# Kernel tuning notes

Hardware: AMD Instinct MI355X
Metric: run time of the kernel (lower is better)

The kernel has to match this reference:

```python
import jax, jax.numpy as jnp
import numpy as np

N = 50000
E = 800000
IN_DIM = 128
HID = 32
HEADS = 8
OUT_DIM = 64
BN_EPS = 1e-5
NEG_SLOPE = 0.2


def batch_norm(x, gamma, beta, mean, var):
    # eval-mode BatchNorm1d using running statistics
    return (x - mean) * jax.lax.rsqrt(var + BN_EPS) * gamma + beta


def gat_conv(x, src, dst, W, att_src, att_dst, heads, out_ch, n):
    """PyG GATConv (shared src/dst lin), self-loops already included in src/dst.
    x: [n, in]; W: [in, heads*out_ch]; att_*: [heads, out_ch].
    Returns [n, heads, out_ch]."""
    h = (x @ W).reshape(n, heads, out_ch)                       # node features per head
    a_s = jnp.einsum('nho,ho->nh', h, att_src)                  # [n, heads]
    a_d = jnp.einsum('nho,ho->nh', h, att_dst)
    e = jax.nn.leaky_relu(a_s[src] + a_d[dst], NEG_SLOPE)       # [e, heads]
    # segment softmax over incoming edges of each dst node
    mx = jax.ops.segment_max(e, dst, num_segments=n)
    ex = jnp.exp(e - mx[dst])
    denom = jax.ops.segment_sum(ex, dst, num_segments=n)
    alpha = ex / (denom[dst] + 1e-16)                           # [e, heads]
    out = jax.ops.segment_sum(alpha[:, :, None] * h[src], dst, num_segments=n)
    return out                                                  # [n, heads, out_ch]


def setup_inputs() -> dict:
    key = jax.random.key(0)
    ks = jax.random.split(key, 24)
    inp = {}
    inp['x'] = jax.random.normal(ks[0], (N, IN_DIM), dtype=jnp.float32)
    inp['edge_index'] = jax.random.randint(ks[1], (2, E), 0, N, dtype=jnp.int64)
    s = 0.05
    inp['W1'] = jax.random.normal(ks[2], (IN_DIM, HEADS * HID), dtype=jnp.float32) * s
    inp['a_src1'] = jax.random.normal(ks[3], (HEADS, HID), dtype=jnp.float32) * s
    inp['a_dst1'] = jax.random.normal(ks[4], (HEADS, HID), dtype=jnp.float32) * s
    inp['b1'] = jnp.zeros((HEADS * HID,), dtype=jnp.float32)
    inp['W2'] = jax.random.normal(ks[5], (HEADS * HID, OUT_DIM), dtype=jnp.float32) * s
    inp['a_src2'] = jax.random.normal(ks[6], (1, OUT_DIM), dtype=jnp.float32) * s
    inp['a_dst2'] = jax.random.normal(ks[7], (1, OUT_DIM), dtype=jnp.float32) * s
    inp['b2'] = jnp.zeros((OUT_DIM,), dtype=jnp.float32)
    # projection Linear(out_dim -> in_dim)
    inp['Wp'] = jax.random.normal(ks[8], (OUT_DIM, IN_DIM), dtype=jnp.float32) * s
    inp['bp'] = jnp.zeros((IN_DIM,), dtype=jnp.float32)
    # BatchNorm params (eval mode running stats)
    for i, d in [(1, HEADS * HID), (2, OUT_DIM), (3, IN_DIM)]:
        k0, k1, k2, k3 = jax.random.split(ks[8 + i], 4)
        inp[f'g{i}'] = 1.0 + 0.1 * jax.random.normal(k0, (d,), dtype=jnp.float32)
        inp[f'be{i}'] = 0.1 * jax.random.normal(k1, (d,), dtype=jnp.float32)
        inp[f'm{i}'] = 0.1 * jax.random.normal(k2, (d,), dtype=jnp.float32)
        inp[f'v{i}'] = jax.random.uniform(k3, (d,), dtype=jnp.float32, minval=0.5, maxval=1.5)
    return inp


def reference(x, edge_index, W1, a_src1, a_dst1, b1, W2, a_src2, a_dst2, b2,
              Wp, bp, g1, be1, m1, v1, g2, be2, m2, v2, g3, be3, m3, v3):
    n = x.shape[0]
    loops = jnp.arange(n, dtype=edge_index.dtype)
    src = jnp.concatenate([edge_index[0], loops])   # add_self_loops=True (PyG default)
    dst = jnp.concatenate([edge_index[1], loops])

    h = gat_conv(x, src, dst, W1, a_src1, a_dst1, HEADS, HID, n)
    h = h.reshape(n, HEADS * HID) + b1              # concat=True
    h = jax.nn.elu(batch_norm(h, g1, be1, m1, v1))  # dropout is no-op in eval

    h = gat_conv(h, src, dst, W2, a_src2, a_dst2, 1, OUT_DIM, n)
    h = h.reshape(n, OUT_DIM) + b2                  # concat=False, heads=1 -> mean == identity
    h = jax.nn.elu(batch_norm(h, g2, be2, m2, v2))

    h = h @ Wp + bp
    return batch_norm(h, g3, be3, m3, v3)
```

## Files before the change

### kernel.cpp

```cpp
#include <hip/hip_runtime.h>
#include <math.h>

#define NEG_SLOPE 0.2f
#define BN_EPS 1e-5f

typedef __bf16 bf16x8 __attribute__((ext_vector_type(8)));
typedef float  f32x4  __attribute__((ext_vector_type(4)));

__device__ __forceinline__ float elu_f(float x){ return x > 0.f ? x : expm1f(x); }
__device__ __forceinline__ float lrelu_f(float x){ return x > 0.f ? x : NEG_SLOPE * x; }

__device__ __forceinline__ float b2f(ushort u){
    union { uint i; float f; } v; v.i = (uint)u << 16; return v.f;
}
__device__ __forceinline__ ushort f2b(float f){
    union { float f; uint i; } v; v.f = f;
    uint r = v.i + 0x7FFFu + ((v.i >> 16) & 1u);
    return (ushort)(r >> 16);
}

__device__ __forceinline__ bool detect_f64(const void* ei, int E, long long N)
{
    const long long* p = (const long long*)ei;
    int lane = threadIdx.x & 63;
    long long v = p[lane % max(1, min(2 * E, 64))];
    bool bad = (v < 0 || v >= N);
    return __ballot(bad) == 0ull;
}

__device__ __forceinline__ void get_edge(const void* ei, int e, int E, bool f64, int& s, int& d)
{
    if (e < E) {
        if (f64) { const long long* p = (const long long*)ei; s = (int)p[e]; d = (int)p[E + e]; }
        else     { const int*       p = (const int*)ei;       s = p[e];      d = p[E + e]; }
    } else {
        s = d = e - E;
    }
}

__global__ void setup_kernel(const void* ei, int E, int N, int* deg, int cx,
    const float* __restrict__ x, ushort* __restrict__ xb,
    const float* __restrict__ W1, const float* __restrict__ W2, const float* __restrict__ Wp,
    ushort* __restrict__ wt1, ushort* __restrict__ wt2, ushort* __restrict__ wtp,
    const float* b1, const float* b2, const float* bp,
    const float* g1, const float* be1, const float* m1, const float* v1,
    const float* g2, const float* be2, const float* m2, const float* v2,
    const float* g3, const float* be3, const float* m3, const float* v3,
    float* par)
{
    int b = blockIdx.x, t = threadIdx.x;
    if (b == 0) {
        { float s = g1[t] * rsqrtf(v1[t] + BN_EPS); par[t] = s;        par[256 + t] = b1[t] * s + be1[t] - m1[t] * s; }
        if (t < 64)  { float s = g2[t] * rsqrtf(v2[t] + BN_EPS); par[512 + t] = s;  par[576 + t] = b2[t] * s + be2[t] - m2[t] * s; }
        if (t < 128) { float s = g3[t] * rsqrtf(v3[t] + BN_EPS); par[640 + t] = s;  par[768 + t] = bp[t] * s + be3[t] - m3[t] * s; }
    } else if (b <= 224) {
        int idx = (b - 1) * 256 + t;
        if (idx < 32768) {
            int n = idx >> 7, k = idx & 127;
            wt1[idx] = f2b(W1[k * 256 + n]);
        } else if (idx < 49152) {
            int j = idx - 32768;
            int n = j >> 8, k = j & 255;
            wt2[j] = f2b(W2[k * 64 + n]);
        } else if (idx < 57344) {
            int j = idx - 49152;
            int n = j >> 6, k = j & 63;
            wtp[j] = f2b(Wp[k * 128 + n]);
        }
    } else if (b < 225 + cx) {
        long long n128 = (long long)N * 128;
        long long idx = ((long long)(b - 225) * 256 + t) * 8;
        if (idx + 7 < n128) {
            float4 v0 = *reinterpret_cast<const float4*>(&x[idx]);
            float4 v1 = *reinterpret_cast<const float4*>(&x[idx + 4]);
            ushort o[8] = { f2b(v0.x), f2b(v0.y), f2b(v0.z), f2b(v0.w),
                            f2b(v1.x), f2b(v1.y), f2b(v1.z), f2b(v1.w) };
            uint4 pk;
            pk.x = (uint)o[0] | ((uint)o[1] << 16);
            pk.y = (uint)o[2] | ((uint)o[3] << 16);
            pk.z = (uint)o[4] | ((uint)o[5] << 16);
            pk.w = (uint)o[6] | ((uint)o[7] << 16);
            *reinterpret_cast<uint4*>(&xb[idx]) = pk;
        } else {
            for (long long q = idx; q < n128; ++q) xb[q] = f2b(x[q]);
        }
    } else {
        bool f64 = detect_f64(ei, E, (long long)N);
        int i = (b - 225 - cx) * 256 + t;
        int ET = E + N;
        if (i < ET) {
            int s, d;
            get_edge(ei, i, E, f64, s, d);
            atomicAdd(&deg[d], 1);
        }
    }
}

__global__ void scan1_kernel(const int* __restrict__ deg, int N, int* __restrict__ bsum)
{
    int b = blockIdx.x, t = threadIdx.x;
    int base = b * 4096 + t * 16;
    int s = 0;
    #pragma unroll
    for (int k = 0; k < 16; k += 4) {
        int idx = base + k;
        if (idx + 3 < N) {
            int4 v = *reinterpret_cast<const int4*>(&deg[idx]);
            s += v.x + v.y + v.z + v.w;
        } else {
            for (int q = 0; q < 4; ++q) if (idx + q < N) s += deg[idx + q];
        }
    }
    #pragma unroll
    for (int off = 1; off < 64; off <<= 1) s += __shfl_xor(s, off);
    __shared__ int wsum[4];
    if ((t & 63) == 0) wsum[t >> 6] = s;
    __syncthreads();
    if (t == 0) bsum[b] = wsum[0] + wsum[1] + wsum[2] + wsum[3];
}

__global__ void scan2_kernel(const int* __restrict__ bsum, int nb, int* __restrict__ bpre)
{
    if (threadIdx.x == 0) {
        int r = 0;
        for (int i = 0; i < nb; ++i) { bpre[i] = r; r += bsum[i]; }
        bpre[nb] = r;
    }
}

__global__ void scan3_kernel(const int* __restrict__ deg, int N,
                             const int* __restrict__ bpre, int nb,
                             int* __restrict__ rowptr, int* __restrict__ fillptr)
{
    int b = blockIdx.x, t = threadIdx.x;
    int base = b * 4096 + t * 16;
    int loc[16];
    int s = 0;
    #pragma unroll
    for (int k = 0; k < 16; ++k) {
        int idx = base + k;
        int d = (idx < N) ? deg[idx] : 0;
        loc[k] = s; s += d;
    }
    int lane = t & 63;
    int incl = s;
    #pragma unroll
    for (int off = 1; off < 64; off <<= 1) {
        int v = __shfl_up(incl, off);
        if (lane >= off) incl += v;
    }
    __shared__ int wsum[4];
    if (lane == 63) wsum[t >> 6] = incl;
    __syncthreads();
    int woff = 0;
    int w = t >> 6;
    for (int i = 0; i < w; ++i) woff += wsum[i];
    int off0 = bpre[b] + woff + incl - s;
    #pragma unroll
    for (int k = 0; k < 16; ++k) {
        int idx = base + k;
        if (idx < N) { rowptr[idx] = off0 + loc[k]; fillptr[idx] = off0 + loc[k]; }
    }
    if (b == 0 && t == 0) rowptr[N] = bpre[nb];
}

__global__ void fill_kernel(const void* ei, int E, int N, int* fillptr, int* esrc)
{
    bool f64 = detect_f64(ei, E, (long long)N);
    int i = blockIdx.x * blockDim.x + threadIdx.x;
    int ET = E + N;
    if (i >= ET) return;
    int s, d;
    get_edge(ei, i, E, f64, s, d);
    int pos = atomicAdd(&fillptr[d], 1);
    esrc[pos] = s;
}

__global__ void prefill_kernel(const char* __restrict__ base, int N, int NS)
{
    int k = blockIdx.x & 7;
    int s = k & (NS - 1);
    int g = blockIdx.x >> 3;
    int ngrp = gridDim.x >> 3;
    size_t slab = (size_t)N * 64;
    size_t per = (slab + ngrp - 1) / ngrp;
    size_t b0 = (size_t)g * per;
    size_t b1 = b0 + per; if (b1 > slab) b1 = slab;
    const char* p = base + (size_t)s * slab;
    uint acc = 0;
    for (size_t o = b0 + (size_t)threadIdx.x * 16; o < b1; o += (size_t)blockDim.x * 16) {
        uint4 v = *reinterpret_cast<const uint4*>(p + o);
        acc ^= v.x ^ v.y ^ v.z ^ v.w;
    }
    asm volatile("" :: "v"(acc));
}

template<int ATYPE, int OMODE, int ATT>
__global__ __launch_bounds__(256) void mgemm_kernel(const void* __restrict__ Ap,
    const ushort* __restrict__ Bt, void* __restrict__ Cp, int M, int K, int NC,
    const float* __restrict__ S, const float* __restrict__ Cc,
    const float* __restrict__ att_s, const float* __restrict__ att_d,
    float* __restrict__ as_out, float* __restrict__ ad_out)
{
    const int BM = 128, LDA = 72;
    __shared__ __align__(16) ushort As[BM][LDA];
    __shared__ __align__(16) ushort Bs[64][LDA];
    __shared__ float red[128][2];
    int t = threadIdx.x;
    int m0 = blockIdx.x * BM, n0 = blockIdx.y * 64;
    int w = t >> 6, l = t & 63;
    int wm = w >> 1, wn = w & 1;
    int r16 = l & 15, kg = l >> 4;

    f32x4 acc[4][2];
    #pragma unroll
    for (int mi = 0; mi < 4; ++mi)
        #pragma unroll
        for (int ni = 0; ni < 2; ++ni)
            acc[mi][ni] = (f32x4){0.f, 0.f, 0.f, 0.f};

    for (int kb = 0; kb < K; kb += 64) {
        if (ATYPE == 0) {
            const float* A = (const float*)Ap;
            #pragma unroll
            for (int p = 0; p < 8; ++p) {
                int r = (t >> 4) + p * 16, c4 = (t & 15) * 4;
                int gm = m0 + r;
                float4 v = (gm < M) ? *reinterpret_cast<const float4*>(&A[(size_t)gm * K + kb + c4])
                                    : make_float4(0.f, 0.f, 0.f, 0.f);
                ushort4 u; u.x = f2b(v.x); u.y = f2b(v.y); u.z = f2b(v.z); u.w = f2b(v.w);
                *reinterpret_cast<ushort4*>(&As[r][c4]) = u;
            }
        } else {
            const ushort* A = (const ushort*)Ap;
            #pragma unroll
            for (int p = 0; p < 4; ++p) {
                int r = (t >> 3) + p * 32, c8 = (t & 7) * 8;
                int gm = m0 + r;
                uint4 v = (gm < M) ? *reinterpret_cast<const uint4*>(&A[(size_t)gm * K + kb + c8])
                                   : make_uint4(0u, 0u, 0u, 0u);
                *reinterpret_cast<uint4*>(&As[r][c8]) = v;
            }
        }
        #pragma unroll
        for (int p = 0; p < 2; ++p) {
            int r = (t >> 3) + p * 32, c8 = (t & 7) * 8;
            uint4 v = *reinterpret_cast<const uint4*>(&Bt[(size_t)(n0 + r) * K + kb + c8]);
            *reinterpret_cast<uint4*>(&Bs[r][c8]) = v;
        }
        __syncthreads();
        #pragma unroll
        for (int kk = 0; kk < 2; ++kk) {
            bf16x8 bB[2], bA[4];
            #pragma unroll
            for (int ni = 0; ni < 2; ++ni)
                bB[ni] = *reinterpret_cast<const bf16x8*>(&Bs[wn * 32 + ni * 16 + r16][kk * 32 + kg * 8]);
            #pragma unroll
            for (int mi = 0; mi < 4; ++mi)
                bA[mi] = *reinterpret_cast<const bf16x8*>(&As[wm * 64 + mi * 16 + r16][kk * 32 + kg * 8]);
            #pragma unroll
            for (int mi = 0; mi < 4; ++mi)
                #pragma unroll
                for (int ni = 0; ni < 2; ++ni)
                    acc[mi][ni] = __builtin_amdgcn_mfma_f32_16x16x32_bf16(bA[mi], bB[ni], acc[mi][ni], 0, 0, 0);
        }
        __syncthreads();
    }
    #pragma unroll
    for (int mi = 0; mi < 4; ++mi) {
        #pragma unroll
        for (int ni = 0; ni < 2; ++ni) {
            #pragma unroll
            for (int rg = 0; rg < 4; ++rg) {
                int gm = m0 + wm * 64 + mi * 16 + kg * 4 + rg;
                int gc = n0 + wn * 32 + ni * 16 + r16;
                if (gm < M) {
                    float v = acc[mi][ni][rg];
                    if (OMODE == 0) {
                        size_t idx = (ATT >= 1)
                            ? ((size_t)(gc >> 5) * M + gm) * 32 + (gc & 31)
                            : (size_t)gm * NC + gc;
                        ((ushort*)Cp)[idx] = f2b(v);
                    } else {
                        ((float*)Cp)[(size_t)gm * NC + gc] = v * S[gc] + Cc[gc];
                    }
                }
            }
        }
    }
    if (ATT) {
        float cs0 = att_s[n0 + wn * 32 + r16], cs1 = att_s[n0 + wn * 32 + 16 + r16];
        float cd0 = att_d[n0 + wn * 32 + r16], cd1 = att_d[n0 + wn * 32 + 16 + r16];
        float sp[4][4], dp[4][4];
        #pragma unroll
        for (int mi = 0; mi < 4; ++mi)
            #pragma unroll
            for (int rg = 0; rg < 4; ++rg) {
                sp[mi][rg] = acc[mi][0][rg] * cs0 + acc[mi][1][rg] * cs1;
                dp[mi][rg] = acc[mi][0][rg] * cd0 + acc[mi][1][rg] * cd1;
            }
        #pragma unroll
        for (int off = 1; off < 16; off <<= 1)
            #pragma unroll
            for (int mi = 0; mi < 4; ++mi)
                #pragma unroll
                for (int rg = 0; rg < 4; ++rg) {
                    sp[mi][rg] += __shfl_xor(sp[mi][rg], off);
                    dp[mi][rg] += __shfl_xor(dp[mi][rg], off);
                }
        if (ATT == 1) {
            int head = (n0 >> 5) + wn;
            if (r16 == 0) {
                #pragma unroll
                for (int mi = 0; mi < 4; ++mi)
                    #pragma unroll
                    for (int rg = 0; rg < 4; ++rg) {
                        int gm = m0 + wm * 64 + mi * 16 + kg * 4 + rg;
                        if (gm < M) {
                            as_out[(size_t)head * M + gm] = sp[mi][rg];
                            ad_out[(size_t)head * M + gm] = dp[mi][rg];
                        }
                    }
            }
        } else {
            if (wn == 1 && r16 == 0) {
                #pragma unroll
                for (int mi = 0; mi < 4; ++mi)
                    #pragma unroll
                    for (int rg = 0; rg < 4; ++rg) {
                        int r = wm * 64 + mi * 16 + kg * 4 + rg;
                        red[r][0] = sp[mi][rg];
                        red[r][1] = dp[mi][rg];
                    }
            }
            __syncthreads();
            if (wn == 0 && r16 == 0) {
                #pragma unroll
                for (int mi = 0; mi < 4; ++mi)
                    #pragma unroll
                    for (int rg = 0; rg < 4; ++rg) {
                        int r = wm * 64 + mi * 16 + kg * 4 + rg;
                        int gm = m0 + r;
                        if (gm < M) {
                            as_out[gm] = sp[mi][rg] + red[r][0];
                            ad_out[gm] = dp[mi][rg] + red[r][1];
                        }
                    }
            }
        }
    }
}

template<int NS, bool SATT>
__global__ void agg_kernel(const ushort* __restrict__ hs,
                           const float* __restrict__ ast, const float* __restrict__ adt,
                           const int* __restrict__ rowptr, const int* __restrict__ esrc,
                           const float* __restrict__ Sv, const float* __restrict__ Cv,
                           ushort* __restrict__ outb, int N)
{
    const int CH = 64;
    __shared__ uint2 wslds[16][CH];
    int s = blockIdx.x & (NS - 1);
    int wslot = threadIdx.x >> 6;
    int lane = threadIdx.x & 63;
    int qq = lane >> 4, li = lane & 15;
    int row = wslot * 4 + qq;
    int n = (int)(blockIdx.x / NS) * 16 + row;
    bool active = (n < N);
    int beg = 0, end = 0;
    float adv = 0.f;
    if (active) {
        beg = rowptr[n];
        end = rowptr[n + 1];
        adv = SATT ? adt[(size_t)s * N + n] : adt[n];
    }
    const float* as_s = SATT ? (ast + (size_t)s * N) : ast;
    const char* slabc = (const char*)(hs + (size_t)s * N * 32);
    int sub = (lane >> 3) & 1;
    uint eoff = (uint)(lane & 7) * 8u;
    float den = 0.f;
    float acc[4] = {0.f, 0.f, 0.f, 0.f};

    for (int cb = beg; cb < end; cb += CH) {
        int cnt = min(CH, end - cb);
        int cnt2 = (cnt + 1) & ~1;
        for (int i = li; i < cnt; i += 16) {
            int src = esrc[cb + i];
            float wv = __expf(lrelu_f(as_s[src] + adv));
            wslds[row][i] = make_uint2(__float_as_uint(wv), (uint)src);
            den += wv;
        }
        if (li == 0 && (cnt & 1)) wslds[row][cnt] = make_uint2(0u, (uint)n);
        __builtin_amdgcn_wave_barrier();
        auto fma4 = [&](uint2 r, float wgt) {
            union { uint u; float f; } c;
            c.u = r.x << 16;         acc[0] += wgt * c.f;
            c.u = r.x & 0xffff0000u; acc[1] += wgt * c.f;
            c.u = r.y << 16;         acc[2] += wgt * c.f;
            c.u = r.y & 0xffff0000u; acc[3] += wgt * c.f;
        };
        int kk = 0;
        for (; kk + 3 < cnt2; kk += 4) {
            uint2 ws0 = wslds[row][kk + sub];
            uint2 ws1 = wslds[row][kk + 2 + sub];
            uint2 r0 = *reinterpret_cast<const uint2*>(slabc + (ws0.y * 64u + eoff));
            uint2 r1 = *reinterpret_cast<const uint2*>(slabc + (ws1.y * 64u + eoff));
            fma4(r0, __uint_as_float(ws0.x));
            fma4(r1, __uint_as_float(ws1.x));
        }
        for (; kk < cnt2; kk += 2) {
            uint2 ws0 = wslds[row][kk + sub];
            uint2 r0 = *reinterpret_cast<const uint2*>(slabc + (ws0.y * 64u + eoff));
            fma4(r0, __uint_as_float(ws0.x));
        }
        __builtin_amdgcn_wave_barrier();
    }

    den += __shfl_xor(den, 1, 64);
    den += __shfl_xor(den, 2, 64);
    den += __shfl_xor(den, 4, 64);
    den += __shfl_xor(den, 8, 64);
    #pragma unroll
    for (int f = 0; f < 4; ++f) acc[f] += __shfl_xor(acc[f], 8, 64);
    if (active && sub == 0) {
        float inv = 1.f / (den + 1e-16f);
        int f = s * 32 + (lane & 7) * 4;
        float4 Sc = *reinterpret_cast<const float4*>(&Sv[f]);
        float4 Cc = *reinterpret_cast<const float4*>(&Cv[f]);
        ushort4 o;
        o.x = f2b(elu_f(acc[0] * inv * Sc.x + Cc.x));
        o.y = f2b(elu_f(acc[1] * inv * Sc.y + Cc.y));
        o.z = f2b(elu_f(acc[2] * inv * Sc.z + Cc.z));
        o.w = f2b(elu_f(acc[3] * inv * Sc.w + Cc.w));
        *reinterpret_cast<ushort4*>(&outb[(size_t)n * (NS * 32) + f]) = o;
    }
}

extern "C" void kernel_launch(void* const* d_in, const int* in_sizes, int n_in,
                              void* d_out, int out_size, void* d_ws, size_t ws_size,
                              hipStream_t stream)
{
    const float* x      = (const float*)d_in[0];
    const void*  ei     = d_in[1];
    const float* W1     = (const float*)d_in[2];
    const float* a_src1 = (const float*)d_in[3];
    const float* a_dst1 = (const float*)d_in[4];
    const float* b1     = (const float*)d_in[5];
    const float* W2     = (const float*)d_in[6];
    const float* a_src2 = (const float*)d_in[7];
    const float* a_dst2 = (const float*)d_in[8];
    const float* b2     = (const float*)d_in[9];
    const float* Wp     = (const float*)d_in[10];
    const float* bp     = (const float*)d_in[11];
    const float* g1 = (const float*)d_in[12], *be1 = (const float*)d_in[13];
    const float* m1 = (const float*)d_in[14], *v1  = (const float*)d_in[15];
    const float* g2 = (const float*)d_in[16], *be2 = (const float*)d_in[17];
    const float* m2 = (const float*)d_in[18], *v2  = (const float*)d_in[19];
    const float* g3 = (const float*)d_in[20], *be3 = (const float*)d_in[21];
    const float* m3 = (const float*)d_in[22], *v3  = (const float*)d_in[23];
    float* out = (float*)d_out;

    const int N  = in_sizes[0] / 128;
    const int E  = in_sizes[1] / 2;
    const int ET = E + N;

    char* base = (char*)d_ws;
    size_t off = 0;
    auto alloc = [&](size_t bytes) -> char* {
        char* p = base + off;
        off += (bytes + 255) & ~(size_t)255;
        return p;
    };
    float*  par     = (float*)alloc(1024 * 4);
    int*    bsum    = (int*)alloc(256);
    int*    bpre    = (int*)alloc(256);
    int*    rowptr  = (int*)alloc((size_t)(N + 1) * 4);
    int*    fillptr = (int*)alloc((size_t)(N + 1) * 4);
    int*    esrc    = (int*)alloc((size_t)ET * 4);
    float*  as1     = (float*)alloc((size_t)N * 8 * 4);
    float*  ad1     = (float*)alloc((size_t)N * 8 * 4);
    float*  as2     = (float*)alloc((size_t)N * 4);
    float*  ad2     = (float*)alloc((size_t)N * 4);
    ushort* wt1     = (ushort*)alloc(256 * 128 * 2);
    ushort* wt2     = (ushort*)alloc(64 * 256 * 2);
    ushort* wtp     = (ushort*)alloc(128 * 64 * 2);
    ushort* xb      = (ushort*)alloc((size_t)N * 128 * 2);
    ushort* h1      = (ushort*)alloc((size_t)N * 256 * 2);
    ushort* h1b     = (ushort*)alloc((size_t)N * 256 * 2);
    ushort* h2      = (ushort*)alloc((size_t)N * 64 * 2);
    ushort* g2buf   = (ushort*)alloc((size_t)N * 64 * 2);

    hipMemsetAsync(fillptr, 0, (N + 1) * sizeof(int), stream);
    int cx = (int)(((size_t)N * 128 + 2047) / 2048);
    int cblocks = (ET + 255) / 256;
    setup_kernel<<<225 + cx + cblocks, 256, 0, stream>>>(ei, E, N, fillptr, cx,
        x, xb, W1, W2, Wp, wt1, wt2, wtp,
        b1, b2, bp, g1, be1, m1, v1, g2, be2, m2, v2, g3, be3, m3, v3, par);

    int nb = (N + 4095) / 4096;
    scan1_kernel<<<nb, 256, 0, stream>>>(fillptr, N, bsum);
    scan2_kernel<<<1, 64, 0, stream>>>(bsum, nb, bpre);
    scan3_kernel<<<nb, 256, 0, stream>>>(fillptr, N, bpre, nb, rowptr, fillptr);
    fill_kernel<<<cblocks, 256, 0, stream>>>(ei, E, N, fillptr, esrc);

    int mb128 = (N + 127) / 128;
    int ngrp16 = (N + 15) / 16;
    mgemm_kernel<1, 0, 1><<<dim3(mb128, 4), 256, 0, stream>>>(xb, wt1, h1, N, 128, 256,
        nullptr, nullptr, a_src1, a_dst1, as1, ad1);
    prefill_kernel<<<512, 256, 0, stream>>>((const char*)h1, N, 8);
    agg_kernel<8, true><<<ngrp16 * 8, 256, 0, stream>>>(h1, as1, ad1, rowptr, esrc,
        par, par + 256, h1b, N);

    mgemm_kernel<1, 0, 2><<<dim3(mb128, 1), 256, 0, stream>>>(h1b, wt2, h2, N, 256, 64,
        nullptr, nullptr, a_src2, a_dst2, as2, ad2);
    prefill_kernel<<<512, 256, 0, stream>>>((const char*)h2, N, 2);
    agg_kernel<2, false><<<ngrp16 * 2, 256, 0, stream>>>(h2, as2, ad2, rowptr, esrc,
        par + 512, par + 576, g2buf, N);

    mgemm_kernel<1, 1, 0><<<dim3(mb128, 2), 256, 0, stream>>>(g2buf, wtp, out, N, 64, 128,
        par + 640, par + 768, nullptr, nullptr, nullptr, nullptr);
}
```

Before: 291.9 us.

## Fuse edge-weight computation into gather loop and drop L2 prefill kernels

```diff
diff --git a/kernel.cpp b/kernel.cpp
--- a/kernel.cpp
+++ b/kernel.cpp
@@ -174,25 +174,6 @@
     get_edge(ei, i, E, f64, s, d);
     int pos = atomicAdd(&fillptr[d], 1);
     esrc[pos] = s;
-}
-
-__global__ void prefill_kernel(const char* __restrict__ base, int N, int NS)
-{
-    int k = blockIdx.x & 7;
-    int s = k & (NS - 1);
-    int g = blockIdx.x >> 3;
-    int ngrp = gridDim.x >> 3;
-    size_t slab = (size_t)N * 64;
-    size_t per = (slab + ngrp - 1) / ngrp;
-    size_t b0 = (size_t)g * per;
-    size_t b1 = b0 + per; if (b1 > slab) b1 = slab;
-    const char* p = base + (size_t)s * slab;
-    uint acc = 0;
-    for (size_t o = b0 + (size_t)threadIdx.x * 16; o < b1; o += (size_t)blockDim.x * 16) {
-        uint4 v = *reinterpret_cast<const uint4*>(p + o);
-        acc ^= v.x ^ v.y ^ v.z ^ v.w;
-    }
-    asm volatile("" :: "v"(acc));
 }
 
 template<int ATYPE, int OMODE, int ATT>
@@ -358,12 +339,10 @@
                            const float* __restrict__ Sv, const float* __restrict__ Cv,
                            ushort* __restrict__ outb, int N)
 {
-    const int CH = 64;
-    __shared__ uint2 wslds[16][CH];
     int s = blockIdx.x & (NS - 1);
     int wslot = threadIdx.x >> 6;
     int lane = threadIdx.x & 63;
-    int qq = lane >> 4, li = lane & 15;
+    int qq = lane >> 4;
     int row = wslot * 4 + qq;
     int n = (int)(blockIdx.x / NS) * 16 + row;
     bool active = (n < N);
@@ -381,39 +360,31 @@
     float den = 0.f;
     float acc[4] = {0.f, 0.f, 0.f, 0.f};
 
-    for (int cb = beg; cb < end; cb += CH) {
-        int cnt = min(CH, end - cb);
-        int cnt2 = (cnt + 1) & ~1;
-        for (int i = li; i < cnt; i += 16) {
-            int src = esrc[cb + i];
-            float wv = __expf(lrelu_f(as_s[src] + adv));
-            wslds[row][i] = make_uint2(__float_as_uint(wv), (uint)src);
-            den += wv;
-        }
-        if (li == 0 && (cnt & 1)) wslds[row][cnt] = make_uint2(0u, (uint)n);
-        __builtin_amdgcn_wave_barrier();
-        auto fma4 = [&](uint2 r, float wgt) {
-            union { uint u; float f; } c;
-            c.u = r.x << 16;         acc[0] += wgt * c.f;
-            c.u = r.x & 0xffff0000u; acc[1] += wgt * c.f;
-            c.u = r.y << 16;         acc[2] += wgt * c.f;
-            c.u = r.y & 0xffff0000u; acc[3] += wgt * c.f;
-        };
-        int kk = 0;
-        for (; kk + 3 < cnt2; kk += 4) {
-            uint2 ws0 = wslds[row][kk + sub];
-            uint2 ws1 = wslds[row][kk + 2 + sub];
-            uint2 r0 = *reinterpret_cast<const uint2*>(slabc + (ws0.y * 64u + eoff));
-            uint2 r1 = *reinterpret_cast<const uint2*>(slabc + (ws1.y * 64u + eoff));
-            fma4(r0, __uint_as_float(ws0.x));
-            fma4(r1, __uint_as_float(ws1.x));
-        }
-        for (; kk < cnt2; kk += 2) {
-            uint2 ws0 = wslds[row][kk + sub];
-            uint2 r0 = *reinterpret_cast<const uint2*>(slabc + (ws0.y * 64u + eoff));
-            fma4(r0, __uint_as_float(ws0.x));
-        }
-        __builtin_amdgcn_wave_barrier();
+    auto body = [&](float av, uint2 r) {
+        float w = __expf(lrelu_f(av + adv));
+        den += w;
+        union { uint u; float f; } c;
+        c.u = r.x << 16;         acc[0] += w * c.f;
+        c.u = r.x & 0xffff0000u; acc[1] += w * c.f;
+        c.u = r.y << 16;         acc[2] += w * c.f;
+        c.u = r.y & 0xffff0000u; acc[3] += w * c.f;
+    };
+
+    int e = beg + sub;
+    for (; e + 6 < end; e += 8) {
+        int s0 = esrc[e], s1 = esrc[e + 2], s2 = esrc[e + 4], s3 = esrc[e + 6];
+        float a0 = as_s[s0], a1 = as_s[s1], a2 = as_s[s2], a3 = as_s[s3];
+        uint2 r0 = *reinterpret_cast<const uint2*>(slabc + ((uint)s0 * 64u + eoff));
+        uint2 r1 = *reinterpret_cast<const uint2*>(slabc + ((uint)s1 * 64u + eoff));
+        uint2 r2 = *reinterpret_cast<const uint2*>(slabc + ((uint)s2 * 64u + eoff));
+        uint2 r3 = *reinterpret_cast<const uint2*>(slabc + ((uint)s3 * 64u + eoff));
+        body(a0, r0); body(a1, r1); body(a2, r2); body(a3, r3);
+    }
+    for (; e < end; e += 2) {
+        int s0 = esrc[e];
+        float a0 = as_s[s0];
+        uint2 r0 = *reinterpret_cast<const uint2*>(slabc + ((uint)s0 * 64u + eoff));
+        body(a0, r0);
     }
 
     den += __shfl_xor(den, 1, 64);
@@ -423,7 +394,7 @@
     #pragma unroll
     for (int f = 0; f < 4; ++f) acc[f] += __shfl_xor(acc[f], 8, 64);
     if (active && sub == 0) {
-        float inv = 1.f / (den + 1e-16f);
+        float inv = 8.f / (den + 8e-16f);
         int f = s * 32 + (lane & 7) * 4;
         float4 Sc = *reinterpret_cast<const float4*>(&Sv[f]);
         float4 Cc = *reinterpret_cast<const float4*>(&Cv[f]);
@@ -507,13 +478,11 @@
     int ngrp16 = (N + 15) / 16;
     mgemm_kernel<1, 0, 1><<<dim3(mb128, 4), 256, 0, stream>>>(xb, wt1, h1, N, 128, 256,
         nullptr, nullptr, a_src1, a_dst1, as1, ad1);
-    prefill_kernel<<<512, 256, 0, stream>>>((const char*)h1, N, 8);
     agg_kernel<8, true><<<ngrp16 * 8, 256, 0, stream>>>(h1, as1, ad1, rowptr, esrc,
         par, par + 256, h1b, N);
 
     mgemm_kernel<1, 0, 2><<<dim3(mb128, 1), 256, 0, stream>>>(h1b, wt2, h2, N, 256, 64,
         nullptr, nullptr, a_src2, a_dst2, as2, ad2);
-    prefill_kernel<<<512, 256, 0, stream>>>((const char*)h2, N, 2);
     agg_kernel<2, false><<<ngrp16 * 2, 256, 0, stream>>>(h2, as2, ad2, rowptr, esrc,
         par + 512, par + 576, g2buf, N);
 
```

New measurement: 280.6 us. -3.9%, faster.
